# Optimization experiments

Hardware: AMD Instinct MI355X
Metric: run time of the kernel (lower is better)

The kernel has to match this reference:

```python
import jax, jax.numpy as jnp
import numpy as np

N_NODES = 50000
N_EDGES = 800000
IN_DIM, HID_DIM, OUT_DIM = 256, 256, 128


def gcn_conv(x, edge_index, W, b, num_nodes):
    """PyG GCNConv: self-loops + symmetric norm + linear + scatter-add + bias."""
    loop = jnp.arange(num_nodes, dtype=edge_index.dtype)
    src = jnp.concatenate([edge_index[0], loop])  # message sources
    dst = jnp.concatenate([edge_index[1], loop])  # message targets
    ones = jnp.ones(dst.shape[0], dtype=x.dtype)
    deg = jax.ops.segment_sum(ones, dst, num_segments=num_nodes)
    dinv = jnp.where(deg > 0, jax.lax.rsqrt(deg), 0.0)
    norm = dinv[src] * dinv[dst]                  # [E+N]
    h = x @ W                                     # [N, out]
    msg = h[src] * norm[:, None]                  # gather + scale, [E+N, out]
    out = jax.ops.segment_sum(msg, dst, num_segments=num_nodes)
    return out + b


def setup_inputs() -> dict:
    key = jax.random.key(0)
    k1, k2, k3, k4, k5, k6 = jax.random.split(key, 6)
    x = jax.random.normal(k1, (N_NODES, IN_DIM), dtype=jnp.float32)
    edge_index = jax.random.randint(k2, (2, N_EDGES), 0, N_NODES, dtype=jnp.int64)
    s1 = 1.0 / np.sqrt(IN_DIM)
    s2 = 1.0 / np.sqrt(HID_DIM)
    W1 = jax.random.uniform(k3, (IN_DIM, HID_DIM), jnp.float32, -s1, s1)
    b1 = jax.random.uniform(k4, (HID_DIM,), jnp.float32, -s1, s1)
    W2 = jax.random.uniform(k5, (HID_DIM, OUT_DIM), jnp.float32, -s2, s2)
    b2 = jax.random.uniform(k6, (OUT_DIM,), jnp.float32, -s2, s2)
    return {"x": x, "edge_index": edge_index, "W1": W1, "b1": b1, "W2": W2, "b2": b2}


def reference(x, edge_index, W1, b1, W2, b2):
    n = x.shape[0]
    h = jax.nn.relu(gcn_conv(x, edge_index, W1, b1, n))
    out = jax.nn.sigmoid(gcn_conv(h, edge_index, W2, b2, n))
    return out
```

## Files before the change

kernel.cpp:

```cpp
#include <hip/hip_runtime.h>
#include <hip/hip_bf16.h>
#include <math.h>

#define N_NODES 50000
#define N_EDGES 800000
#define D_IN 256
#define D_HID 256
#define D_OUT 128

typedef unsigned short ushort_t;
typedef unsigned char uchar_t;
typedef __attribute__((ext_vector_type(8))) short bf16x8;
typedef __attribute__((ext_vector_type(4))) float f32x4;

__device__ inline ushort_t f2bf(float f) {
    __hip_bfloat16 h = __float2bfloat16(f);
    return *reinterpret_cast<ushort_t*>(&h);
}
__device__ inline float blo(unsigned u) {
    union { unsigned i; float f; } v; v.i = u << 16; return v.f;
}
__device__ inline float bhi(unsigned u) {
    union { unsigned i; float f; } v; v.i = u & 0xffff0000u; return v.f;
}
__device__ inline uchar_t f2fp8(float a) {
    int w = __builtin_amdgcn_cvt_pk_fp8_f32(a, a, 0, false);
    return (uchar_t)(w & 0xff);
}
__device__ inline void fp8x4_to_f32(unsigned u, float* o) {
    auto p0 = __builtin_amdgcn_cvt_pk_f32_fp8(u, false);
    auto p1 = __builtin_amdgcn_cvt_pk_f32_fp8(u, true);
    o[0] = p0[0]; o[1] = p0[1]; o[2] = p1[0]; o[3] = p1[1];
}


__global__ __launch_bounds__(256) void k_count_convW(const int* __restrict__ dst,
                                                     int* __restrict__ degI,
                                                     const float* __restrict__ W1,
                                                     const float* __restrict__ W2,
                                                     ushort_t* __restrict__ Wt1,
                                                     ushort_t* __restrict__ Wt2,
                                                     uchar_t* __restrict__ h1z,
                                                     ushort_t* __restrict__ h2z) {
    const int b = blockIdx.x;
    if (b < 3125) {
        int i = b * 256 + threadIdx.x;
        if (i < N_EDGES) atomicAdd(&degI[dst[i]], 1);
    } else {
        int i = (b - 3125) * 256 + threadIdx.x;
        const int n1 = D_IN * D_HID;
        const int n2 = D_HID * D_OUT;
        if (i < n1) {
            int k = i / D_HID, n = i % D_HID;
            Wt1[(size_t)n * D_IN + k] = f2bf(W1[i]);
        } else if (i < n1 + n2) {
            int j = i - n1;
            int k = j / D_OUT, n = j % D_OUT;
            Wt2[(size_t)n * D_HID + k] = f2bf(W2[j]);
        } else {
            int j = i - n1 - n2;
            if (j < D_HID) h1z[j] = 0;
            else if (j < D_HID + D_OUT) h2z[j - D_HID] = 0;
        }
    }
}


__global__ __launch_bounds__(256) void k_scan_apply(const int* __restrict__ degI,
                                                    int* __restrict__ offs,
                                                    int* __restrict__ cursor,
                                                    float* __restrict__ dinv,
                                                    int* __restrict__ ebuf, int n) {
    __shared__ int s[256];
    const int t = threadIdx.x;
    const int b = blockIdx.x;

    int pre = 0;
    const int lim = b * 256;
    for (int i = t; i < lim; i += 256) pre += (degI[i] + 15) & ~15;
    s[t] = pre;
    __syncthreads();
    for (int st = 128; st > 0; st >>= 1) {
        if (t < st) s[t] += s[t + st];
        __syncthreads();
    }
    const int blockoff = s[0];
    __syncthreads();

    const int i = b * 256 + t;
    const int deg = (i < n) ? degI[i] : 0;
    const int v = (deg + 15) & ~15;
    s[t] = v;
    __syncthreads();
    for (int off = 1; off < 256; off <<= 1) {
        int u = 0;
        if (t >= off) u = s[t - off];
        __syncthreads();
        if (t >= off) s[t] += u;
        __syncthreads();
    }
    const int excl = s[t] - v + blockoff;
    if (i < n) {
        offs[i] = excl;
        cursor[i] = excl;
        dinv[i] = rsqrtf((float)(1 + deg));
        for (int p = excl + deg; p < excl + v; ++p) ebuf[p] = N_NODES;
        if (i == n - 1) offs[n] = excl + v;
    }
}

__global__ void k_fill(const int* __restrict__ src, const int* __restrict__ dst,
                       int* __restrict__ cursor, int* __restrict__ ebuf, int e) {
    int i = blockIdx.x * 256 + threadIdx.x;
    if (i < e) {
        int d = dst[i];
        int pos = atomicAdd(&cursor[d], 1);
        ebuf[pos] = src[i];
    }
}


__global__ __launch_bounds__(512) void k_gemm1(const float* __restrict__ A,
                                               const ushort_t* __restrict__ Bt,
                                               const float* __restrict__ dinvD,
                                               uchar_t* __restrict__ C, int M) {
    __shared__ ushort_t As[128 * 40];
    __shared__ ushort_t Bs[256 * 40];

    const int t = threadIdx.x;
    const int lane = t & 63;
    const int w = t >> 6;
    const int wr = w >> 2;
    const int wc = w & 3;
    const int m0 = blockIdx.x * 128;

    const int arow = t >> 2;
    const int acol = (t & 3) * 8;
    const int brow = t >> 1;
    const int bcol = (t & 1) * 16;

    f32x4 acc[4][4];
#pragma unroll
    for (int m = 0; m < 4; ++m)
#pragma unroll
        for (int n = 0; n < 4; ++n)
#pragma unroll
            for (int i = 0; i < 4; ++i) acc[m][n][i] = 0.0f;

    for (int kt = 0; kt < 256; kt += 32) {
        {
            const int gr = m0 + arow;
            float4 v0 = make_float4(0.f, 0.f, 0.f, 0.f);
            float4 v1 = make_float4(0.f, 0.f, 0.f, 0.f);
            if (gr < M) {
                const float* p = A + (size_t)gr * 256 + kt + acol;
                v0 = *(const float4*)p;
                v1 = *(const float4*)(p + 4);
            }
            ushort4 u0, u1;
            u0.x = f2bf(v0.x); u0.y = f2bf(v0.y); u0.z = f2bf(v0.z); u0.w = f2bf(v0.w);
            u1.x = f2bf(v1.x); u1.y = f2bf(v1.y); u1.z = f2bf(v1.z); u1.w = f2bf(v1.w);
            *(ushort4*)&As[arow * 40 + acol] = u0;
            *(ushort4*)&As[arow * 40 + acol + 4] = u1;
        }
        {
            const uint4* p = (const uint4*)(Bt + (size_t)brow * 256 + kt + bcol);
            uint4 v0 = p[0], v1 = p[1];
            *(uint4*)&Bs[brow * 40 + bcol] = v0;
            *(uint4*)&Bs[brow * 40 + bcol + 8] = v1;
        }
        __syncthreads();

        const int kg = (lane >> 4) * 8;
        const int lr = lane & 15;
        bf16x8 a[4], b[4];
#pragma unroll
        for (int m = 0; m < 4; ++m)
            a[m] = *(const bf16x8*)&As[(wr * 64 + m * 16 + lr) * 40 + kg];
#pragma unroll
        for (int n = 0; n < 4; ++n)
            b[n] = *(const bf16x8*)&Bs[(wc * 64 + n * 16 + lr) * 40 + kg];
#pragma unroll
        for (int m = 0; m < 4; ++m)
#pragma unroll
            for (int n = 0; n < 4; ++n)
                acc[m][n] = __builtin_amdgcn_mfma_f32_16x16x32_bf16(a[m], b[n], acc[m][n], 0, 0, 0);
        __syncthreads();
    }

    const int lr = lane & 15;
    const int rg = (lane >> 4) * 4;
#pragma unroll
    for (int m = 0; m < 4; ++m) {
        const int rb = m0 + wr * 64 + m * 16 + rg;
#pragma unroll
        for (int i = 0; i < 4; ++i) {
            const int row = rb + i;
            if (row < M) {
                const float dr = dinvD[row];
#pragma unroll
                for (int n = 0; n < 4; ++n) {
                    const int col = wc * 64 + n * 16 + lr;
                    C[(size_t)row * 256 + col] = f2fp8(acc[m][n][i] * dr);
                }
            }
        }
    }
}


__global__ __launch_bounds__(256) void k_gemm2(const ushort_t* __restrict__ A,
                                               const ushort_t* __restrict__ Bt,
                                               const float* __restrict__ dinvD,
                                               ushort_t* __restrict__ C, int M) {
    __shared__ ushort_t As[128 * 40];
    __shared__ ushort_t Bs[128 * 40];

    const int t = threadIdx.x;
    const int lane = t & 63;
    const int w = t >> 6;
    const int wr = w >> 1, wc = w & 1;
    const int m0 = blockIdx.x * 128;

    const int srow = t >> 1;
    const int scol = (t & 1) * 16;

    f32x4 acc[4][4];
#pragma unroll
    for (int m = 0; m < 4; ++m)
#pragma unroll
        for (int n = 0; n < 4; ++n)
#pragma unroll
            for (int i = 0; i < 4; ++i) acc[m][n][i] = 0.0f;

    for (int kt = 0; kt < 256; kt += 32) {
        {
            const int gr = m0 + srow;
            uint4 v0 = make_uint4(0, 0, 0, 0), v1 = make_uint4(0, 0, 0, 0);
            if (gr < M) {
                const uint4* p = (const uint4*)(A + (size_t)gr * 256 + kt + scol);
                v0 = p[0]; v1 = p[1];
            }
            *(uint4*)&As[srow * 40 + scol] = v0;
            *(uint4*)&As[srow * 40 + scol + 8] = v1;
        }
        {
            const uint4* p = (const uint4*)(Bt + (size_t)srow * 256 + kt + scol);
            uint4 v0 = p[0], v1 = p[1];
            *(uint4*)&Bs[srow * 40 + scol] = v0;
            *(uint4*)&Bs[srow * 40 + scol + 8] = v1;
        }
        __syncthreads();

        const int kg = (lane >> 4) * 8;
        const int lr = lane & 15;
        bf16x8 a[4], b[4];
#pragma unroll
        for (int m = 0; m < 4; ++m)
            a[m] = *(const bf16x8*)&As[(wr * 64 + m * 16 + lr) * 40 + kg];
#pragma unroll
        for (int n = 0; n < 4; ++n)
            b[n] = *(const bf16x8*)&Bs[(wc * 64 + n * 16 + lr) * 40 + kg];
#pragma unroll
        for (int m = 0; m < 4; ++m)
#pragma unroll
            for (int n = 0; n < 4; ++n)
                acc[m][n] = __builtin_amdgcn_mfma_f32_16x16x32_bf16(a[m], b[n], acc[m][n], 0, 0, 0);
        __syncthreads();
    }

    const int lr = lane & 15;
    const int rg = (lane >> 4) * 4;
#pragma unroll
    for (int m = 0; m < 4; ++m) {
        const int rb = m0 + wr * 64 + m * 16 + rg;
#pragma unroll
        for (int i = 0; i < 4; ++i) {
            const int row = rb + i;
            if (row < M) {
                const float dr = dinvD[row];
#pragma unroll
                for (int n = 0; n < 4; ++n) {
                    const int col = wc * 64 + n * 16 + lr;
                    C[(size_t)row * 128 + col] = f2bf(acc[m][n][i] * dr);
                }
            }
        }
    }
}


__device__ inline void ld_idx16(const int* __restrict__ p, int* s) {
    int4 a = ((const int4*)p)[0];
    int4 b = ((const int4*)p)[1];
    int4 c = ((const int4*)p)[2];
    int4 d = ((const int4*)p)[3];
    s[0]  = __builtin_amdgcn_readfirstlane(a.x);
    s[1]  = __builtin_amdgcn_readfirstlane(a.y);
    s[2]  = __builtin_amdgcn_readfirstlane(a.z);
    s[3]  = __builtin_amdgcn_readfirstlane(a.w);
    s[4]  = __builtin_amdgcn_readfirstlane(b.x);
    s[5]  = __builtin_amdgcn_readfirstlane(b.y);
    s[6]  = __builtin_amdgcn_readfirstlane(b.z);
    s[7]  = __builtin_amdgcn_readfirstlane(b.w);
    s[8]  = __builtin_amdgcn_readfirstlane(c.x);
    s[9]  = __builtin_amdgcn_readfirstlane(c.y);
    s[10] = __builtin_amdgcn_readfirstlane(c.z);
    s[11] = __builtin_amdgcn_readfirstlane(c.w);
    s[12] = __builtin_amdgcn_readfirstlane(d.x);
    s[13] = __builtin_amdgcn_readfirstlane(d.y);
    s[14] = __builtin_amdgcn_readfirstlane(d.z);
    s[15] = __builtin_amdgcn_readfirstlane(d.w);
}


__global__ __launch_bounds__(256) void k_gather_fp8(const uchar_t* __restrict__ h,
                                                    const float* __restrict__ dinv,
                                                    const int* __restrict__ offs,
                                                    const int* __restrict__ ebuf,
                                                    const float* __restrict__ bias,
                                                    ushort_t* __restrict__ out, int n) {
    const int node = (blockIdx.x * 256 + threadIdx.x) >> 6;
    const int lane = threadIdx.x & 63;
    if (node >= n) return;

    const int base = lane * 4;
    const uchar_t* hb = h + base;
    const float di = dinv[node];

    float acc[4];
    {
        const unsigned u = *(const unsigned*)(hb + (size_t)node * D_HID);
        fp8x4_to_f32(u, acc);
    }

    int e = __builtin_amdgcn_readfirstlane(offs[node]);
    const int e1 = __builtin_amdgcn_readfirstlane(offs[node + 1]);

    int cs[16], ns[16];
    bool have = e < e1;
    if (have) ld_idx16(ebuf + e, cs);

    while (have) {
        const int en = e + 16;
        const bool hn = en < e1;
        unsigned u[16];
#pragma unroll
        for (int j = 0; j < 16; ++j)
            u[j] = *(const unsigned*)(hb + (size_t)cs[j] * D_HID);
        if (hn) ld_idx16(ebuf + en, ns);
#pragma unroll
        for (int j = 0; j < 16; ++j) {
            float d[4];
            fp8x4_to_f32(u[j], d);
            acc[0] += d[0]; acc[1] += d[1]; acc[2] += d[2]; acc[3] += d[3];
        }
        e = en; have = hn;
#pragma unroll
        for (int j = 0; j < 16; ++j) cs[j] = ns[j];
    }

    ushort4 o;
    o.x = f2bf(fmaxf(di * acc[0] + bias[base + 0], 0.f));
    o.y = f2bf(fmaxf(di * acc[1] + bias[base + 1], 0.f));
    o.z = f2bf(fmaxf(di * acc[2] + bias[base + 2], 0.f));
    o.w = f2bf(fmaxf(di * acc[3] + bias[base + 3], 0.f));
    *(ushort4*)(out + (size_t)node * D_HID + base) = o;
}


__global__ __launch_bounds__(256) void k_gather_bf2(const ushort_t* __restrict__ h,
                                                    const float* __restrict__ dinv,
                                                    const int* __restrict__ offs,
                                                    const int* __restrict__ ebuf,
                                                    const float* __restrict__ bias,
                                                    float* __restrict__ out, int n) {
    const int node = (blockIdx.x * 256 + threadIdx.x) >> 6;
    const int lane = threadIdx.x & 63;
    if (node >= n) return;

    const int base = lane * 2;
    const ushort_t* hb = h + base;
    const float di = dinv[node];

    float acc[2];
    {
        unsigned u = *(const unsigned*)(hb + (size_t)node * D_OUT);
        acc[0] = blo(u); acc[1] = bhi(u);
    }

    int e = __builtin_amdgcn_readfirstlane(offs[node]);
    const int e1 = __builtin_amdgcn_readfirstlane(offs[node + 1]);

    int cs[16], ns[16];
    bool have = e < e1;
    if (have) ld_idx16(ebuf + e, cs);

    while (have) {
        const int en = e + 16;
        const bool hn = en < e1;
        unsigned u[16];
#pragma unroll
        for (int j = 0; j < 16; ++j)
            u[j] = *(const unsigned*)(hb + (size_t)cs[j] * D_OUT);
        if (hn) ld_idx16(ebuf + en, ns);
#pragma unroll
        for (int j = 0; j < 16; ++j) {
            acc[0] += blo(u[j]); acc[1] += bhi(u[j]);
        }
        e = en; have = hn;
#pragma unroll
        for (int j = 0; j < 16; ++j) cs[j] = ns[j];
    }

    const float v0 = di * acc[0] + bias[base + 0];
    const float v1 = di * acc[1] + bias[base + 1];
    float2 r;
    r.x = 1.0f / (1.0f + expf(-v0));
    r.y = 1.0f / (1.0f + expf(-v1));
    *(float2*)(out + (size_t)node * D_OUT + base) = r;
}


extern "C" void kernel_launch(void* const* d_in, const int* in_sizes, int n_in,
                              void* d_out, int out_size, void* d_ws, size_t ws_size,
                              hipStream_t stream) {
    const float* x  = (const float*)d_in[0];
    const int*   ei = (const int*)d_in[1];
    const float* W1 = (const float*)d_in[2];
    const float* b1 = (const float*)d_in[3];
    const float* W2 = (const float*)d_in[4];
    const float* b2 = (const float*)d_in[5];
    float* out = (float*)d_out;

    float* wsf    = (float*)d_ws;
    float* dinv   = wsf;
    int*   degI   = (int*)(wsf + 50048);
    int*   offs   = degI + 50048;
    int*   cursor = offs + 50064;
    int*   ebuf   = cursor + 50048;
    ushort_t* Wt1 = (ushort_t*)(ebuf + 1600000);
    ushort_t* Wt2 = Wt1 + 65536;
    uchar_t*  h1  = (uchar_t*)(Wt2 + 32768);
    ushort_t* agg1= (ushort_t*)(h1 + (size_t)50048 * D_HID);
    ushort_t* h2  = agg1 + (size_t)50048 * D_HID;

    const int* src = ei;
    const int* dst = ei + N_EDGES;

    const int blocksN = (N_NODES + 255) / 256;

    hipMemsetAsync(degI, 0, N_NODES * sizeof(int), stream);

    k_count_convW<<<3125 + 386, 256, 0, stream>>>(dst, degI, W1, W2, Wt1, Wt2,
                                                  h1 + (size_t)N_NODES * D_HID,
                                                  h2 + (size_t)N_NODES * D_OUT);

    k_scan_apply<<<blocksN, 256, 0, stream>>>(degI, offs, cursor, dinv, ebuf, N_NODES);

    k_fill<<<(N_EDGES + 255) / 256, 256, 0, stream>>>(src, dst, cursor, ebuf, N_EDGES);

    k_gemm1<<<(N_NODES + 127) / 128, 512, 0, stream>>>(x, Wt1, dinv, h1, N_NODES);

    k_gather_fp8<<<(N_NODES * 64 + 255) / 256, 256, 0, stream>>>(
        h1, dinv, offs, ebuf, b1, agg1, N_NODES);

    k_gemm2<<<(N_NODES + 127) / 128, 256, 0, stream>>>(agg1, Wt2, dinv, h2, N_NODES);

    k_gather_bf2<<<(N_NODES * 64 + 255) / 256, 256, 0, stream>>>(
        h2, dinv, offs, ebuf, b2, out, N_NODES);
}
```

Measured before the change: 236.7 us.

## Compress edge indices to u16, store h2 as fp8, fuse fill with gemm1

Stores the CSR source indices as 16-bit values, which halves index traffic in both gathers, and stores the second-layer features h2 in fp8 instead of bf16, which halves gather bandwidth in the last layer. The edge fill kernel is merged into the gemm1 launch as extra blocks so the two independent stages can overlap and one launch is removed. The u16 indices hold because node count is below 65536. fp8 for h2 adds quantization error to the output, and fusing the fill into 512-thread gemm blocks leaves the unused shared-memory allocation on those blocks.

```diff
diff --git a/kernel.cpp b/kernel.cpp
--- a/kernel.cpp
+++ b/kernel.cpp
@@ -31,6 +31,10 @@
     auto p0 = __builtin_amdgcn_cvt_pk_f32_fp8(u, false);
     auto p1 = __builtin_amdgcn_cvt_pk_f32_fp8(u, true);
     o[0] = p0[0]; o[1] = p0[1]; o[2] = p1[0]; o[3] = p1[1];
+}
+__device__ inline void fp8x2_to_f32(unsigned u, float* o) {
+    auto p0 = __builtin_amdgcn_cvt_pk_f32_fp8(u, false);
+    o[0] = p0[0]; o[1] = p0[1];
 }
 
 
@@ -41,7 +45,7 @@
                                                      ushort_t* __restrict__ Wt1,
                                                      ushort_t* __restrict__ Wt2,
                                                      uchar_t* __restrict__ h1z,
-                                                     ushort_t* __restrict__ h2z) {
+                                                     uchar_t* __restrict__ h2z) {
     const int b = blockIdx.x;
     if (b < 3125) {
         int i = b * 256 + threadIdx.x;
@@ -70,7 +74,7 @@
                                                     int* __restrict__ offs,
                                                     int* __restrict__ cursor,
                                                     float* __restrict__ dinv,
-                                                    int* __restrict__ ebuf, int n) {
+                                                    ushort_t* __restrict__ ebuf, int n) {
     __shared__ int s[256];
     const int t = threadIdx.x;
     const int b = blockIdx.x;
@@ -104,28 +108,33 @@
         offs[i] = excl;
         cursor[i] = excl;
         dinv[i] = rsqrtf((float)(1 + deg));
-        for (int p = excl + deg; p < excl + v; ++p) ebuf[p] = N_NODES;
+        for (int p = excl + deg; p < excl + v; ++p) ebuf[p] = (ushort_t)N_NODES;
         if (i == n - 1) offs[n] = excl + v;
     }
 }
 
-__global__ void k_fill(const int* __restrict__ src, const int* __restrict__ dst,
-                       int* __restrict__ cursor, int* __restrict__ ebuf, int e) {
-    int i = blockIdx.x * 256 + threadIdx.x;
-    if (i < e) {
-        int d = dst[i];
-        int pos = atomicAdd(&cursor[d], 1);
-        ebuf[pos] = src[i];
-    }
-}
-
-
-__global__ __launch_bounds__(512) void k_gemm1(const float* __restrict__ A,
-                                               const ushort_t* __restrict__ Bt,
-                                               const float* __restrict__ dinvD,
-                                               uchar_t* __restrict__ C, int M) {
+
+__global__ __launch_bounds__(512) void k_fill_gemm1(const int* __restrict__ src,
+                                                    const int* __restrict__ dst,
+                                                    int* __restrict__ cursor,
+                                                    ushort_t* __restrict__ ebuf,
+                                                    const float* __restrict__ A,
+                                                    const ushort_t* __restrict__ Bt,
+                                                    const float* __restrict__ dinvD,
+                                                    uchar_t* __restrict__ C,
+                                                    int M, int gemmBlocks) {
     __shared__ ushort_t As[128 * 40];
     __shared__ ushort_t Bs[256 * 40];
+
+    if (blockIdx.x >= gemmBlocks) {
+        const int i = (blockIdx.x - gemmBlocks) * 512 + threadIdx.x;
+        if (i < N_EDGES) {
+            const int d = dst[i];
+            const int pos = atomicAdd(&cursor[d], 1);
+            ebuf[pos] = (ushort_t)src[i];
+        }
+        return;
+    }
 
     const int t = threadIdx.x;
     const int lane = t & 63;
@@ -212,7 +221,7 @@
 __global__ __launch_bounds__(256) void k_gemm2(const ushort_t* __restrict__ A,
                                                const ushort_t* __restrict__ Bt,
                                                const float* __restrict__ dinvD,
-                                               ushort_t* __restrict__ C, int M) {
+                                               uchar_t* __restrict__ C, int M) {
     __shared__ ushort_t As[128 * 40];
     __shared__ ushort_t Bs[128 * 40];
 
@@ -282,7 +291,7 @@
 #pragma unroll
                 for (int n = 0; n < 4; ++n) {
                     const int col = wc * 64 + n * 16 + lr;
-                    C[(size_t)row * 128 + col] = f2bf(acc[m][n][i] * dr);
+                    C[(size_t)row * 128 + col] = f2fp8(acc[m][n][i] * dr);
                 }
             }
         }
@@ -290,34 +299,32 @@
 }
 
 
-__device__ inline void ld_idx16(const int* __restrict__ p, int* s) {
-    int4 a = ((const int4*)p)[0];
-    int4 b = ((const int4*)p)[1];
-    int4 c = ((const int4*)p)[2];
-    int4 d = ((const int4*)p)[3];
-    s[0]  = __builtin_amdgcn_readfirstlane(a.x);
-    s[1]  = __builtin_amdgcn_readfirstlane(a.y);
-    s[2]  = __builtin_amdgcn_readfirstlane(a.z);
-    s[3]  = __builtin_amdgcn_readfirstlane(a.w);
-    s[4]  = __builtin_amdgcn_readfirstlane(b.x);
-    s[5]  = __builtin_amdgcn_readfirstlane(b.y);
-    s[6]  = __builtin_amdgcn_readfirstlane(b.z);
-    s[7]  = __builtin_amdgcn_readfirstlane(b.w);
-    s[8]  = __builtin_amdgcn_readfirstlane(c.x);
-    s[9]  = __builtin_amdgcn_readfirstlane(c.y);
-    s[10] = __builtin_amdgcn_readfirstlane(c.z);
-    s[11] = __builtin_amdgcn_readfirstlane(c.w);
-    s[12] = __builtin_amdgcn_readfirstlane(d.x);
-    s[13] = __builtin_amdgcn_readfirstlane(d.y);
-    s[14] = __builtin_amdgcn_readfirstlane(d.z);
-    s[15] = __builtin_amdgcn_readfirstlane(d.w);
+__device__ inline void ld_idx16u(const ushort_t* __restrict__ p, int* s) {
+    uint4 a = ((const uint4*)p)[0];
+    uint4 b = ((const uint4*)p)[1];
+    unsigned w0 = __builtin_amdgcn_readfirstlane(a.x);
+    unsigned w1 = __builtin_amdgcn_readfirstlane(a.y);
+    unsigned w2 = __builtin_amdgcn_readfirstlane(a.z);
+    unsigned w3 = __builtin_amdgcn_readfirstlane(a.w);
+    unsigned w4 = __builtin_amdgcn_readfirstlane(b.x);
+    unsigned w5 = __builtin_amdgcn_readfirstlane(b.y);
+    unsigned w6 = __builtin_amdgcn_readfirstlane(b.z);
+    unsigned w7 = __builtin_amdgcn_readfirstlane(b.w);
+    s[0]  = w0 & 0xffff; s[1]  = w0 >> 16;
+    s[2]  = w1 & 0xffff; s[3]  = w1 >> 16;
+    s[4]  = w2 & 0xffff; s[5]  = w2 >> 16;
+    s[6]  = w3 & 0xffff; s[7]  = w3 >> 16;
+    s[8]  = w4 & 0xffff; s[9]  = w4 >> 16;
+    s[10] = w5 & 0xffff; s[11] = w5 >> 16;
+    s[12] = w6 & 0xffff; s[13] = w6 >> 16;
+    s[14] = w7 & 0xffff; s[15] = w7 >> 16;
 }
 
 
 __global__ __launch_bounds__(256) void k_gather_fp8(const uchar_t* __restrict__ h,
                                                     const float* __restrict__ dinv,
                                                     const int* __restrict__ offs,
-                                                    const int* __restrict__ ebuf,
+                                                    const ushort_t* __restrict__ ebuf,
                                                     const float* __restrict__ bias,
                                                     ushort_t* __restrict__ out, int n) {
     const int node = (blockIdx.x * 256 + threadIdx.x) >> 6;
@@ -339,7 +346,7 @@
 
     int cs[16], ns[16];
     bool have = e < e1;
-    if (have) ld_idx16(ebuf + e, cs);
+    if (have) ld_idx16u(ebuf + e, cs);
 
     while (have) {
         const int en = e + 16;
@@ -348,7 +355,7 @@
 #pragma unroll
         for (int j = 0; j < 16; ++j)
             u[j] = *(const unsigned*)(hb + (size_t)cs[j] * D_HID);
-        if (hn) ld_idx16(ebuf + en, ns);
+        if (hn) ld_idx16u(ebuf + en, ns);
 #pragma unroll
         for (int j = 0; j < 16; ++j) {
             float d[4];
@@ -369,24 +376,24 @@
 }
 
 
-__global__ __launch_bounds__(256) void k_gather_bf2(const ushort_t* __restrict__ h,
-                                                    const float* __restrict__ dinv,
-                                                    const int* __restrict__ offs,
-                                                    const int* __restrict__ ebuf,
-                                                    const float* __restrict__ bias,
-                                                    float* __restrict__ out, int n) {
+__global__ __launch_bounds__(256) void k_gather_fp8_2(const uchar_t* __restrict__ h,
+                                                      const float* __restrict__ dinv,
+                                                      const int* __restrict__ offs,
+                                                      const ushort_t* __restrict__ ebuf,
+                                                      const float* __restrict__ bias,
+                                                      float* __restrict__ out, int n) {
     const int node = (blockIdx.x * 256 + threadIdx.x) >> 6;
     const int lane = threadIdx.x & 63;
     if (node >= n) return;
 
     const int base = lane * 2;
-    const ushort_t* hb = h + base;
+    const uchar_t* hb = h + base;
     const float di = dinv[node];
 
     float acc[2];
     {
-        unsigned u = *(const unsigned*)(hb + (size_t)node * D_OUT);
-        acc[0] = blo(u); acc[1] = bhi(u);
+        const unsigned u = *(const ushort_t*)(hb + (size_t)node * D_OUT);
+        fp8x2_to_f32(u, acc);
     }
 
     int e = __builtin_amdgcn_readfirstlane(offs[node]);
@@ -394,7 +401,7 @@
 
     int cs[16], ns[16];
     bool have = e < e1;
-    if (have) ld_idx16(ebuf + e, cs);
+    if (have) ld_idx16u(ebuf + e, cs);
 
     while (have) {
         const int en = e + 16;
@@ -402,11 +409,13 @@
         unsigned u[16];
 #pragma unroll
         for (int j = 0; j < 16; ++j)
-            u[j] = *(const unsigned*)(hb + (size_t)cs[j] * D_OUT);
-        if (hn) ld_idx16(ebuf + en, ns);
+            u[j] = *(const ushort_t*)(hb + (size_t)cs[j] * D_OUT);
+        if (hn) ld_idx16u(ebuf + en, ns);
 #pragma unroll
         for (int j = 0; j < 16; ++j) {
-            acc[0] += blo(u[j]); acc[1] += bhi(u[j]);
+            float d[2];
+            fp8x2_to_f32(u[j], d);
+            acc[0] += d[0]; acc[1] += d[1];
         }
         e = en; have = hn;
 #pragma unroll
@@ -438,12 +447,12 @@
     int*   degI   = (int*)(wsf + 50048);
     int*   offs   = degI + 50048;
     int*   cursor = offs + 50064;
-    int*   ebuf   = cursor + 50048;
-    ushort_t* Wt1 = (ushort_t*)(ebuf + 1600000);
+    ushort_t* ebuf= (ushort_t*)(cursor + 50048);
+    ushort_t* Wt1 = ebuf + 1600000;
     ushort_t* Wt2 = Wt1 + 65536;
     uchar_t*  h1  = (uchar_t*)(Wt2 + 32768);
     ushort_t* agg1= (ushort_t*)(h1 + (size_t)50048 * D_HID);
-    ushort_t* h2  = agg1 + (size_t)50048 * D_HID;
+    uchar_t*  h2  = (uchar_t*)(agg1 + (size_t)50048 * D_HID);
 
     const int* src = ei;
     const int* dst = ei + N_EDGES;
@@ -458,15 +467,18 @@
 
     k_scan_apply<<<blocksN, 256, 0, stream>>>(degI, offs, cursor, dinv, ebuf, N_NODES);
 
-    k_fill<<<(N_EDGES + 255) / 256, 256, 0, stream>>>(src, dst, cursor, ebuf, N_EDGES);
-
-    k_gemm1<<<(N_NODES + 127) / 128, 512, 0, stream>>>(x, Wt1, dinv, h1, N_NODES);
+    {
+        const int gemmBlocks = (N_NODES + 127) / 128;
+        const int fillBlocks = (N_EDGES + 511) / 512;
+        k_fill_gemm1<<<gemmBlocks + fillBlocks, 512, 0, stream>>>(
+            src, dst, cursor, ebuf, x, Wt1, dinv, h1, N_NODES, gemmBlocks);
+    }
 
     k_gather_fp8<<<(N_NODES * 64 + 255) / 256, 256, 0, stream>>>(
         h1, dinv, offs, ebuf, b1, agg1, N_NODES);
 
     k_gemm2<<<(N_NODES + 127) / 128, 256, 0, stream>>>(agg1, Wt2, dinv, h2, N_NODES);
 
-    k_gather_bf2<<<(N_NODES * 64 + 255) / 256, 256, 0, stream>>>(
+    k_gather_fp8_2<<<(N_NODES * 64 + 255) / 256, 256, 0, stream>>>(
         h2, dinv, offs, ebuf, b2, out, N_NODES);
 }
```

Result: faster. 209.0 us (-11.7%).
